# Kernel tuning notes

Measured on AMD Instinct MI355X. Metric: run time of the kernel, lower is better.

Reference implementation:

```python
import jax, jax.numpy as jnp
import numpy as np

B, S, E, H, Dh = 1, 2048, 1024, 16, 64


def setup_inputs() -> dict:
    key = jax.random.key(0)
    ks = jax.random.split(key, 9)
    sc = 0.02
    return {
        "x": jax.random.normal(ks[0], (B, S, E), jnp.float32),
        "Wq": jax.random.normal(ks[1], (H, E, Dh), jnp.float32) * sc,
        "bq": jax.random.normal(ks[2], (H, Dh), jnp.float32) * sc,
        "Wk": jax.random.normal(ks[3], (H, E, Dh), jnp.float32) * sc,
        "bk": jax.random.normal(ks[4], (H, Dh), jnp.float32) * sc,
        "Wv": jax.random.normal(ks[5], (H, E, Dh), jnp.float32) * sc,
        "bv": jax.random.normal(ks[6], (H, Dh), jnp.float32) * sc,
        "Wo": jax.random.normal(ks[7], (E, E), jnp.float32) * sc,
        "bo": jax.random.normal(ks[8], (E,), jnp.float32) * sc,
    }


def reference(x, Wq, bq, Wk, bk, Wv, bv, Wo, bo):
    # Per-head projections (stacked): [B,S,E] x [H,E,Dh] -> [B,H,S,Dh]
    q = jnp.einsum("bse,hed->bhsd", x, Wq) + bq[None, :, None, :]
    k = jnp.einsum("bse,hed->bhsd", x, Wk) + bk[None, :, None, :]
    v = jnp.einsum("bse,hed->bhsd", x, Wv) + bv[None, :, None, :]
    scores = jnp.einsum("bhsd,bhtd->bhst", q, k) / np.sqrt(Dh).astype(np.float32)
    causal = jnp.tril(jnp.ones((S, S), dtype=bool))  # [S,S]
    scores = jnp.where(causal[None, None], scores, -jnp.inf)
    attn = jax.nn.softmax(scores, axis=-1)  # attn_dropout p=0 -> identity
    out = jnp.einsum("bhst,bhtd->bhsd", attn, v)
    # concat heads in head order: [B,S,H*Dh]
    out = out.transpose(0, 2, 1, 3).reshape(B, S, H * Dh)
    return out @ Wo.T if False else jnp.einsum("bsf,ef->bse", out, Wo.T.T * 0 + Wo) if False else out @ Wo.swapaxes(0, 1) * 0 + (jnp.einsum("bsf,fe->bse", out, Wo) + bo)
```

## Files before the change

### kernel.cpp

```cpp
#include <hip/hip_runtime.h>

#define S_LEN 2048
#define E_DIM 1024
#define NH 16
#define DH 64

typedef __bf16 v8bf __attribute__((ext_vector_type(8)));
typedef float f32x4 __attribute__((ext_vector_type(4)));
typedef unsigned short u16x4 __attribute__((ext_vector_type(4)));
typedef unsigned short u16x8 __attribute__((ext_vector_type(8)));

__device__ __align__(16) unsigned short g_Xb[S_LEN * E_DIM];
__device__ __align__(16) unsigned short g_WT[3 * E_DIM * E_DIM];
__device__ __align__(16) unsigned short g_WoT[E_DIM * E_DIM];
__device__ __align__(16) unsigned short g_Qb[NH * S_LEN * DH];
__device__ __align__(16) unsigned short g_Kb[NH * S_LEN * DH];
__device__ __align__(16) unsigned short g_Vt[NH * DH * S_LEN];
__device__ __align__(16) unsigned short g_AO[S_LEN * E_DIM];

__device__ inline unsigned short f2bf(float f) {
    unsigned int u = __float_as_uint(f);
    u += 0x7FFF + ((u >> 16) & 1);
    return (unsigned short)(u >> 16);
}
__device__ inline f32x4 mfma16(v8bf a, v8bf b, f32x4 c) {
    return __builtin_amdgcn_mfma_f32_16x16x32_bf16(a, b, c, 0, 0, 0);
}
#define SWZ(v, pat) __int_as_float(__builtin_amdgcn_ds_swizzle(__float_as_int(v), (pat)))

typedef __attribute__((address_space(3))) unsigned int lds_u32;
typedef __attribute__((address_space(1))) const unsigned int glb_u32;
__device__ inline void async_cp16(const unsigned short* g, unsigned short* l) {
    __builtin_amdgcn_global_load_lds((glb_u32*)g, (lds_u32*)l, 16, 0, 0);
}

__global__ __launch_bounds__(256) void prep(const float* __restrict__ X,
                                            const float* __restrict__ Wq,
                                            const float* __restrict__ Wk,
                                            const float* __restrict__ Wv,
                                            const float* __restrict__ Wo) {
    __shared__ unsigned short lds[64 * 65];
    int b = blockIdx.x;
    if (b < 2048) {
        int t = b * 256 + threadIdx.x;
        typedef float f4 __attribute__((ext_vector_type(4)));
        f4 v = reinterpret_cast<const f4*>(X)[t];
        u16x4 o = {f2bf(v.x), f2bf(v.y), f2bf(v.z), f2bf(v.w)};
        reinterpret_cast<u16x4*>(g_Xb)[t] = o;
    } else if (b < 2304) {
        int bb = b - 2048;
        const int h = bb >> 4;
        const int e0 = (bb & 15) * 64;
        const float* srcs[3] = {Wq, Wk, Wv};
#pragma unroll
        for (int t = 0; t < 3; t++) {
            const float* W = srcs[t] + h * 65536;
            for (int p = 0; p < 16; p++) {
                int e = p * 4 + (threadIdx.x >> 6);
                int d = threadIdx.x & 63;
                lds[d * 65 + e] = f2bf(W[(e0 + e) * 64 + d]);
            }
            __syncthreads();
            unsigned short* dst = g_WT + (t * 1024 + h * 64) * E_DIM + e0;
            for (int p = 0; p < 16; p++) {
                int d = p * 4 + (threadIdx.x >> 6);
                int e = threadIdx.x & 63;
                dst[d * E_DIM + e] = lds[d * 65 + e];
            }
            __syncthreads();
        }
    } else {
        int bb = b - 2304;
        const int f0 = (bb >> 4) * 64;
        const int e0 = (bb & 15) * 64;
        for (int p = 0; p < 16; p++) {
            int f = p * 4 + (threadIdx.x >> 6);
            int e = threadIdx.x & 63;
            lds[e * 65 + f] = f2bf(Wo[(f0 + f) * E_DIM + e0 + e]);
        }
        __syncthreads();
        for (int p = 0; p < 16; p++) {
            int e = p * 4 + (threadIdx.x >> 6);
            int f = threadIdx.x & 63;
            g_WoT[(e0 + e) * E_DIM + f0 + f] = lds[e * 65 + f];
        }
    }
}

__global__ __launch_bounds__(256) void qkv_gemm(const float* __restrict__ bq,
                                                const float* __restrict__ bk,
                                                const float* __restrict__ bv) {
    __shared__ __align__(16) unsigned short lds[12288];
    unsigned short* lA = lds;
    unsigned short* lB = lds + 4096;
    const int t = threadIdx.x;
    const int wave = t >> 6;
    const int lane = t & 63;
    const int m = lane & 15, quad = lane >> 4;
    const int sHalf = wave >> 1, nHalf = wave & 1;
    const int s0 = blockIdx.x * 64;
    const int n0 = blockIdx.y * 128;

    const int rl = t >> 3;
    const int cx = (t & 7) ^ (rl & 7);

    f32x4 acc[2][4];
#pragma unroll
    for (int i = 0; i < 2; i++)
#pragma unroll
        for (int j = 0; j < 4; j++) acc[i][j] = (f32x4){0.f, 0.f, 0.f, 0.f};

    const int axor = m & 7;
    const unsigned short* lAr0 = lA + (sHalf * 32 + m) * 64;
    const unsigned short* lAr1 = lA + (sHalf * 32 + 16 + m) * 64;
    const unsigned short* lBr  = lB + (nHalf * 64 + m) * 64;

    for (int k0 = 0; k0 < E_DIM; k0 += 64) {
        const unsigned short* ga = g_Xb + (s0 + rl) * E_DIM + k0 + cx * 8;
        async_cp16(ga,              lA + wave * 512);
        async_cp16(ga + 32 * E_DIM, lA + wave * 512 + 2048);
        const unsigned short* gb = g_WT + (n0 + rl) * E_DIM + k0 + cx * 8;
        async_cp16(gb,              lB + wave * 512);
        async_cp16(gb + 32 * E_DIM, lB + wave * 512 + 2048);
        async_cp16(gb + 64 * E_DIM, lB + wave * 512 + 4096);
        async_cp16(gb + 96 * E_DIM, lB + wave * 512 + 6144);
        __syncthreads();
#pragma unroll
        for (int ks = 0; ks < 2; ks++) {
            const int ch = ((ks * 4 + quad) ^ axor) * 8;
            v8bf a0 = *reinterpret_cast<const v8bf*>(lAr0 + ch);
            v8bf a1 = *reinterpret_cast<const v8bf*>(lAr1 + ch);
#pragma unroll
            for (int nt = 0; nt < 4; nt++) {
                v8bf bfr = *reinterpret_cast<const v8bf*>(lBr + nt * 16 * 64 + ch);
                acc[0][nt] = mfma16(a0, bfr, acc[0][nt]);
                acc[1][nt] = mfma16(a1, bfr, acc[1][nt]);
            }
        }
        __syncthreads();
    }

    const int tensor = n0 >> 10;
    const int nn0 = n0 & 1023;
    const float* bb = tensor == 0 ? bq : (tensor == 1 ? bk : bv);
    float bias[4];
#pragma unroll
    for (int nt = 0; nt < 4; nt++) bias[nt] = bb[nn0 + nHalf * 64 + nt * 16 + m];

    if (tensor < 2) {
#pragma unroll
        for (int half = 0; half < 2; half++)
#pragma unroll
            for (int nt = 0; nt < 4; nt++)
#pragma unroll
                for (int r = 0; r < 4; r++) {
                    int sl = sHalf * 32 + half * 16 + quad * 4 + r;
                    int nl = nHalf * 64 + nt * 16 + m;
                    lds[sl * 136 + nl] = f2bf(acc[half][nt][r] + bias[nt]);
                }
        __syncthreads();
        unsigned short* dst = tensor == 0 ? g_Qb : g_Kb;
#pragma unroll
        for (int p = 0; p < 4; p++) {
            int row = p * 16 + (t >> 4);
            int c = t & 15;
            u16x8 v = *reinterpret_cast<const u16x8*>(lds + row * 136 + c * 8);
            int h = (nn0 >> 6) + (c >> 3);
            int d = (c & 7) * 8;
            *reinterpret_cast<u16x8*>(dst + (h * S_LEN + s0 + row) * DH + d) = v;
        }
    } else {
#pragma unroll
        for (int half = 0; half < 2; half++)
#pragma unroll
            for (int nt = 0; nt < 4; nt++)
#pragma unroll
                for (int r = 0; r < 4; r++) {
                    int sl = sHalf * 32 + half * 16 + quad * 4 + r;
                    int nl = nHalf * 64 + nt * 16 + m;
                    lds[nl * 72 + sl] = f2bf(acc[half][nt][r] + bias[nt]);
                }
        __syncthreads();
#pragma unroll
        for (int p = 0; p < 4; p++) {
            int nl = p * 32 + (t >> 3);
            int c = t & 7;
            u16x8 v = *reinterpret_cast<const u16x8*>(lds + nl * 72 + c * 8);
            int nn = nn0 + nl;
            int h = nn >> 6, d = nn & 63;
            *reinterpret_cast<u16x8*>(g_Vt + (h * DH + d) * S_LEN + s0 + c * 8) = v;
        }
    }
}

__global__ __launch_bounds__(64) void flash_attn() {
    __shared__ __align__(16) unsigned short plds[32 * 72];
    const int lane = threadIdx.x;
    const int m = lane & 15, quad = lane >> 4;
    const int h = blockIdx.x & 15;
    const int s0 = (63 - (blockIdx.x >> 4)) * 32;

    const unsigned short* Qh = g_Qb + h * S_LEN * DH;
    const unsigned short* Kh = g_Kb + h * S_LEN * DH;
    const unsigned short* Vh = g_Vt + h * DH * S_LEN;

    v8bf aqA0 = *reinterpret_cast<const v8bf*>(Qh + (s0 + m) * DH + quad * 8);
    v8bf aqA1 = *reinterpret_cast<const v8bf*>(Qh + (s0 + m) * DH + 32 + quad * 8);
    v8bf aqB0 = *reinterpret_cast<const v8bf*>(Qh + (s0 + 16 + m) * DH + quad * 8);
    v8bf aqB1 = *reinterpret_cast<const v8bf*>(Qh + (s0 + 16 + m) * DH + 32 + quad * 8);

    f32x4 oA[4], oB[4];
#pragma unroll
    for (int i = 0; i < 4; i++) { oA[i] = (f32x4){0.f,0.f,0.f,0.f}; oB[i] = (f32x4){0.f,0.f,0.f,0.f}; }
    float lsA[4] = {0.f,0.f,0.f,0.f}, lsB[4] = {0.f,0.f,0.f,0.f};

    const float SC = 0.125f * 1.44269504088896f;

    for (int t0 = 0; t0 < s0 + 32; t0 += 64) {
        v8bf kf[4][2];
#pragma unroll
        for (int ct = 0; ct < 4; ct++) {
            const unsigned short* kp = Kh + (t0 + ct * 16 + m) * DH + quad * 8;
            kf[ct][0] = *reinterpret_cast<const v8bf*>(kp);
            kf[ct][1] = *reinterpret_cast<const v8bf*>(kp + 32);
        }
        f32x4 sA[4], sB[4];
#pragma unroll
        for (int ct = 0; ct < 4; ct++) {
            sA[ct] = (f32x4){0.f,0.f,0.f,0.f};
            sA[ct] = mfma16(aqA0, kf[ct][0], sA[ct]);
            sA[ct] = mfma16(aqA1, kf[ct][1], sA[ct]);
            sB[ct] = (f32x4){0.f,0.f,0.f,0.f};
            sB[ct] = mfma16(aqB0, kf[ct][0], sB[ct]);
            sB[ct] = mfma16(aqB1, kf[ct][1], sB[ct]);
        }
#pragma unroll
        for (int ct = 0; ct < 4; ct++) {
            int colbase = t0 + ct * 16;
            int col = colbase + m;
            if (colbase + 15 > s0) {
#pragma unroll
                for (int r = 0; r < 4; r++)
                    if (col > s0 + quad * 4 + r) sA[ct][r] = -3e38f;
            }
            if (colbase + 15 > s0 + 16) {
#pragma unroll
                for (int r = 0; r < 4; r++)
                    if (col > s0 + 16 + quad * 4 + r) sB[ct][r] = -3e38f;
            }
        }
        v8bf vf[4][2];
#pragma unroll
        for (int dt = 0; dt < 4; dt++) {
            const unsigned short* vp = Vh + (dt * 16 + m) * S_LEN + t0 + quad * 8;
            vf[dt][0] = *reinterpret_cast<const v8bf*>(vp);
            vf[dt][1] = *reinterpret_cast<const v8bf*>(vp + 32);
        }
#pragma unroll
        for (int ct = 0; ct < 4; ct++)
#pragma unroll
            for (int r = 0; r < 4; r++) {
                sA[ct][r] = __builtin_amdgcn_exp2f(sA[ct][r] * SC);
                sB[ct][r] = __builtin_amdgcn_exp2f(sB[ct][r] * SC);
            }
#pragma unroll
        for (int r = 0; r < 4; r++) {
            lsA[r] += (sA[0][r] + sA[1][r]) + (sA[2][r] + sA[3][r]);
            lsB[r] += (sB[0][r] + sB[1][r]) + (sB[2][r] + sB[3][r]);
        }
#pragma unroll
        for (int ct = 0; ct < 4; ct++)
#pragma unroll
            for (int r = 0; r < 4; r++) {
                plds[(quad * 4 + r) * 72 + ct * 16 + m]        = f2bf(sA[ct][r]);
                plds[(16 + quad * 4 + r) * 72 + ct * 16 + m]   = f2bf(sB[ct][r]);
            }
        __syncthreads();
        v8bf apA0 = *reinterpret_cast<const v8bf*>(plds + m * 72 + quad * 8);
        v8bf apA1 = *reinterpret_cast<const v8bf*>(plds + m * 72 + 32 + quad * 8);
        v8bf apB0 = *reinterpret_cast<const v8bf*>(plds + (16 + m) * 72 + quad * 8);
        v8bf apB1 = *reinterpret_cast<const v8bf*>(plds + (16 + m) * 72 + 32 + quad * 8);
        __syncthreads();
#pragma unroll
        for (int dt = 0; dt < 4; dt++) {
            oA[dt] = mfma16(apA0, vf[dt][0], oA[dt]);
            oA[dt] = mfma16(apA1, vf[dt][1], oA[dt]);
            oB[dt] = mfma16(apB0, vf[dt][0], oB[dt]);
            oB[dt] = mfma16(apB1, vf[dt][1], oB[dt]);
        }
    }

    float invA[4], invB[4];
#pragma unroll
    for (int r = 0; r < 4; r++) {
        float a = lsA[r], b = lsB[r];
        a += SWZ(a, 0x041F); b += SWZ(b, 0x041F);
        a += SWZ(a, 0x081F); b += SWZ(b, 0x081F);
        a += SWZ(a, 0x101F); b += SWZ(b, 0x101F);
        a += SWZ(a, 0x201F); b += SWZ(b, 0x201F);
        invA[r] = 1.0f / a;  invB[r] = 1.0f / b;
    }
#pragma unroll
    for (int dt = 0; dt < 4; dt++)
#pragma unroll
        for (int r = 0; r < 4; r++) {
            int sA_ = s0 + quad * 4 + r;
            int sB_ = s0 + 16 + quad * 4 + r;
            g_AO[sA_ * E_DIM + h * 64 + dt * 16 + m] = f2bf(oA[dt][r] * invA[r]);
            g_AO[sB_ * E_DIM + h * 64 + dt * 16 + m] = f2bf(oB[dt][r] * invB[r]);
        }
}

__global__ __launch_bounds__(256) void out_gemm(const float* __restrict__ bo,
                                                float* __restrict__ OUT) {
    __shared__ __align__(16) unsigned short lds[12288];
    unsigned short* lA = lds;
    unsigned short* lB = lds + 4096;
    const int t = threadIdx.x;
    const int wave = t >> 6;
    const int lane = t & 63;
    const int m = lane & 15, quad = lane >> 4;
    const int sHalf = wave >> 1, nHalf = wave & 1;
    const int s0 = blockIdx.x * 64;
    const int n0 = blockIdx.y * 128;

    const int rl = t >> 3;
    const int cx = (t & 7) ^ (rl & 7);

    f32x4 acc[2][4];
#pragma unroll
    for (int i = 0; i < 2; i++)
#pragma unroll
        for (int j = 0; j < 4; j++) acc[i][j] = (f32x4){0.f, 0.f, 0.f, 0.f};

    const int axor = m & 7;
    const unsigned short* lAr0 = lA + (sHalf * 32 + m) * 64;
    const unsigned short* lAr1 = lA + (sHalf * 32 + 16 + m) * 64;
    const unsigned short* lBr  = lB + (nHalf * 64 + m) * 64;

    for (int k0 = 0; k0 < E_DIM; k0 += 64) {
        const unsigned short* ga = g_AO + (s0 + rl) * E_DIM + k0 + cx * 8;
        async_cp16(ga,              lA + wave * 512);
        async_cp16(ga + 32 * E_DIM, lA + wave * 512 + 2048);
        const unsigned short* gb = g_WoT + (n0 + rl) * E_DIM + k0 + cx * 8;
        async_cp16(gb,              lB + wave * 512);
        async_cp16(gb + 32 * E_DIM, lB + wave * 512 + 2048);
        async_cp16(gb + 64 * E_DIM, lB + wave * 512 + 4096);
        async_cp16(gb + 96 * E_DIM, lB + wave * 512 + 6144);
        __syncthreads();
#pragma unroll
        for (int ks = 0; ks < 2; ks++) {
            const int ch = ((ks * 4 + quad) ^ axor) * 8;
            v8bf a0 = *reinterpret_cast<const v8bf*>(lAr0 + ch);
            v8bf a1 = *reinterpret_cast<const v8bf*>(lAr1 + ch);
#pragma unroll
            for (int nt = 0; nt < 4; nt++) {
                v8bf bfr = *reinterpret_cast<const v8bf*>(lBr + nt * 16 * 64 + ch);
                acc[0][nt] = mfma16(a0, bfr, acc[0][nt]);
                acc[1][nt] = mfma16(a1, bfr, acc[1][nt]);
            }
        }
        __syncthreads();
    }
#pragma unroll
    for (int half = 0; half < 2; half++)
#pragma unroll
        for (int nt = 0; nt < 4; nt++) {
            int e = n0 + nHalf * 64 + nt * 16 + m;
            float bias = bo[e];
#pragma unroll
            for (int r = 0; r < 4; r++) {
                int s = s0 + sHalf * 32 + half * 16 + quad * 4 + r;
                OUT[s * E_DIM + e] = acc[half][nt][r] + bias;
            }
        }
}

extern "C" void kernel_launch(void* const* d_in, const int* in_sizes, int n_in,
                              void* d_out, int out_size, void* d_ws, size_t ws_size,
                              hipStream_t stream) {
    (void)in_sizes; (void)n_in; (void)out_size; (void)d_ws; (void)ws_size;
    const float* x  = (const float*)d_in[0];
    const float* Wq = (const float*)d_in[1];
    const float* bq = (const float*)d_in[2];
    const float* Wk = (const float*)d_in[3];
    const float* bk = (const float*)d_in[4];
    const float* Wv = (const float*)d_in[5];
    const float* bv = (const float*)d_in[6];
    const float* Wo = (const float*)d_in[7];
    const float* bo = (const float*)d_in[8];
    float* out = (float*)d_out;

    hipLaunchKernelGGL(prep,       dim3(2560),   dim3(256), 0, stream, x, Wq, Wk, Wv, Wo);
    hipLaunchKernelGGL(qkv_gemm,   dim3(32, 24), dim3(256), 0, stream, bq, bk, bv);
    hipLaunchKernelGGL(flash_attn, dim3(1024),   dim3(64),  0, stream);
    hipLaunchKernelGGL(out_gemm,   dim3(32, 8),  dim3(256), 0, stream, bo, out);
}
```

Measured before the change: 184.2 us.

## Split attention KV loop across four waves, enlarge QKV GEMM tile, vectorize prep transposes

The flash attention kernel now runs four waves per block. Each wave handles every fourth 64-key chunk, and the partial outputs and row sums are combined through LDS at the end, which gives more parallelism per query tile. This is valid because the kernel uses a fixed max (exp2 of the scaled score with no running max), so the partials simply add. The QKV GEMM tile grows to 128x128 with 4x4 MFMA fragments per wave for more reuse, and the prep transposes use vectorized loads and stores. The costs are extra LDS use and register pressure, plus fewer QKV blocks.

```diff
diff --git a/kernel.cpp b/kernel.cpp
--- a/kernel.cpp
+++ b/kernel.cpp
@@ -39,33 +39,39 @@
                                             const float* __restrict__ Wk,
                                             const float* __restrict__ Wv,
                                             const float* __restrict__ Wo) {
-    __shared__ unsigned short lds[64 * 65];
-    int b = blockIdx.x;
+    __shared__ __align__(16) unsigned short lds[64 * 72];
+    const int b = blockIdx.x;
+    const int t = threadIdx.x;
     if (b < 2048) {
-        int t = b * 256 + threadIdx.x;
-        typedef float f4 __attribute__((ext_vector_type(4)));
-        f4 v = reinterpret_cast<const f4*>(X)[t];
+        int i = b * 256 + t;
+        f32x4 v = reinterpret_cast<const f32x4*>(X)[i];
         u16x4 o = {f2bf(v.x), f2bf(v.y), f2bf(v.z), f2bf(v.w)};
-        reinterpret_cast<u16x4*>(g_Xb)[t] = o;
+        reinterpret_cast<u16x4*>(g_Xb)[i] = o;
     } else if (b < 2304) {
         int bb = b - 2048;
         const int h = bb >> 4;
         const int e0 = (bb & 15) * 64;
         const float* srcs[3] = {Wq, Wk, Wv};
 #pragma unroll
-        for (int t = 0; t < 3; t++) {
-            const float* W = srcs[t] + h * 65536;
-            for (int p = 0; p < 16; p++) {
-                int e = p * 4 + (threadIdx.x >> 6);
-                int d = threadIdx.x & 63;
-                lds[d * 65 + e] = f2bf(W[(e0 + e) * 64 + d]);
+        for (int tn = 0; tn < 3; tn++) {
+            const float* W = srcs[tn] + h * 65536;
+#pragma unroll
+            for (int p = 0; p < 4; p++) {
+                int e = p * 16 + (t >> 4);
+                int d = (t & 15) * 4;
+                f32x4 v = *reinterpret_cast<const f32x4*>(&W[(e0 + e) * 64 + d]);
+                lds[(d + 0) * 72 + e] = f2bf(v.x);
+                lds[(d + 1) * 72 + e] = f2bf(v.y);
+                lds[(d + 2) * 72 + e] = f2bf(v.z);
+                lds[(d + 3) * 72 + e] = f2bf(v.w);
             }
             __syncthreads();
-            unsigned short* dst = g_WT + (t * 1024 + h * 64) * E_DIM + e0;
-            for (int p = 0; p < 16; p++) {
-                int d = p * 4 + (threadIdx.x >> 6);
-                int e = threadIdx.x & 63;
-                dst[d * E_DIM + e] = lds[d * 65 + e];
+#pragma unroll
+            for (int p = 0; p < 2; p++) {
+                int d = p * 32 + (t >> 3);
+                int ec = (t & 7) * 8;
+                u16x8 o = *reinterpret_cast<const u16x8*>(&lds[d * 72 + ec]);
+                *reinterpret_cast<u16x8*>(&g_WT[(tn * 1024 + h * 64 + d) * E_DIM + e0 + ec]) = o;
             }
             __syncthreads();
         }
@@ -73,16 +79,23 @@
         int bb = b - 2304;
         const int f0 = (bb >> 4) * 64;
         const int e0 = (bb & 15) * 64;
-        for (int p = 0; p < 16; p++) {
-            int f = p * 4 + (threadIdx.x >> 6);
-            int e = threadIdx.x & 63;
-            lds[e * 65 + f] = f2bf(Wo[(f0 + f) * E_DIM + e0 + e]);
-        }
-        __syncthreads();
-        for (int p = 0; p < 16; p++) {
-            int e = p * 4 + (threadIdx.x >> 6);
-            int f = threadIdx.x & 63;
-            g_WoT[(e0 + e) * E_DIM + f0 + f] = lds[e * 65 + f];
+#pragma unroll
+        for (int p = 0; p < 4; p++) {
+            int f = p * 16 + (t >> 4);
+            int e = (t & 15) * 4;
+            f32x4 v = *reinterpret_cast<const f32x4*>(&Wo[(f0 + f) * E_DIM + e0 + e]);
+            lds[(e + 0) * 72 + f] = f2bf(v.x);
+            lds[(e + 1) * 72 + f] = f2bf(v.y);
+            lds[(e + 2) * 72 + f] = f2bf(v.z);
+            lds[(e + 3) * 72 + f] = f2bf(v.w);
+        }
+        __syncthreads();
+#pragma unroll
+        for (int p = 0; p < 2; p++) {
+            int e = p * 32 + (t >> 3);
+            int fc = (t & 7) * 8;
+            u16x8 o = *reinterpret_cast<const u16x8*>(&lds[e * 72 + fc]);
+            *reinterpret_cast<u16x8*>(&g_WoT[(e0 + e) * E_DIM + f0 + fc]) = o;
         }
     }
 }
@@ -90,52 +103,54 @@
 __global__ __launch_bounds__(256) void qkv_gemm(const float* __restrict__ bq,
                                                 const float* __restrict__ bk,
                                                 const float* __restrict__ bv) {
-    __shared__ __align__(16) unsigned short lds[12288];
+    __shared__ __align__(16) unsigned short lds[17408];
     unsigned short* lA = lds;
-    unsigned short* lB = lds + 4096;
+    unsigned short* lB = lds + 8192;
     const int t = threadIdx.x;
     const int wave = t >> 6;
     const int lane = t & 63;
     const int m = lane & 15, quad = lane >> 4;
-    const int sHalf = wave >> 1, nHalf = wave & 1;
-    const int s0 = blockIdx.x * 64;
+    const int s0 = blockIdx.x * 128;
     const int n0 = blockIdx.y * 128;
+    const int wr = (wave >> 1) * 64, wc = (wave & 1) * 64;
 
     const int rl = t >> 3;
     const int cx = (t & 7) ^ (rl & 7);
-
-    f32x4 acc[2][4];
-#pragma unroll
-    for (int i = 0; i < 2; i++)
+    const int axor = m & 7;
+
+    f32x4 acc[4][4];
+#pragma unroll
+    for (int i = 0; i < 4; i++)
 #pragma unroll
         for (int j = 0; j < 4; j++) acc[i][j] = (f32x4){0.f, 0.f, 0.f, 0.f};
-
-    const int axor = m & 7;
-    const unsigned short* lAr0 = lA + (sHalf * 32 + m) * 64;
-    const unsigned short* lAr1 = lA + (sHalf * 32 + 16 + m) * 64;
-    const unsigned short* lBr  = lB + (nHalf * 64 + m) * 64;
 
     for (int k0 = 0; k0 < E_DIM; k0 += 64) {
         const unsigned short* ga = g_Xb + (s0 + rl) * E_DIM + k0 + cx * 8;
         async_cp16(ga,              lA + wave * 512);
-        async_cp16(ga + 32 * E_DIM, lA + wave * 512 + 2048);
+        async_cp16(ga + 32 * E_DIM, lA + 2048 + wave * 512);
+        async_cp16(ga + 64 * E_DIM, lA + 4096 + wave * 512);
+        async_cp16(ga + 96 * E_DIM, lA + 6144 + wave * 512);
         const unsigned short* gb = g_WT + (n0 + rl) * E_DIM + k0 + cx * 8;
         async_cp16(gb,              lB + wave * 512);
-        async_cp16(gb + 32 * E_DIM, lB + wave * 512 + 2048);
-        async_cp16(gb + 64 * E_DIM, lB + wave * 512 + 4096);
-        async_cp16(gb + 96 * E_DIM, lB + wave * 512 + 6144);
+        async_cp16(gb + 32 * E_DIM, lB + 2048 + wave * 512);
+        async_cp16(gb + 64 * E_DIM, lB + 4096 + wave * 512);
+        async_cp16(gb + 96 * E_DIM, lB + 6144 + wave * 512);
         __syncthreads();
 #pragma unroll
         for (int ks = 0; ks < 2; ks++) {
             const int ch = ((ks * 4 + quad) ^ axor) * 8;
-            v8bf a0 = *reinterpret_cast<const v8bf*>(lAr0 + ch);
-            v8bf a1 = *reinterpret_cast<const v8bf*>(lAr1 + ch);
-#pragma unroll
-            for (int nt = 0; nt < 4; nt++) {
-                v8bf bfr = *reinterpret_cast<const v8bf*>(lBr + nt * 16 * 64 + ch);
-                acc[0][nt] = mfma16(a0, bfr, acc[0][nt]);
-                acc[1][nt] = mfma16(a1, bfr, acc[1][nt]);
-            }
+            v8bf a[4], bf[4];
+#pragma unroll
+            for (int i = 0; i < 4; i++)
+                a[i] = *reinterpret_cast<const v8bf*>(lA + (wr + i * 16 + m) * 64 + ch);
+#pragma unroll
+            for (int j = 0; j < 4; j++)
+                bf[j] = *reinterpret_cast<const v8bf*>(lB + (wc + j * 16 + m) * 64 + ch);
+#pragma unroll
+            for (int i = 0; i < 4; i++)
+#pragma unroll
+                for (int j = 0; j < 4; j++)
+                    acc[i][j] = mfma16(a[i], bf[j], acc[i][j]);
         }
         __syncthreads();
     }
@@ -145,57 +160,60 @@
     const float* bb = tensor == 0 ? bq : (tensor == 1 ? bk : bv);
     float bias[4];
 #pragma unroll
-    for (int nt = 0; nt < 4; nt++) bias[nt] = bb[nn0 + nHalf * 64 + nt * 16 + m];
+    for (int j = 0; j < 4; j++) bias[j] = bb[nn0 + wc + j * 16 + m];
 
     if (tensor < 2) {
 #pragma unroll
-        for (int half = 0; half < 2; half++)
-#pragma unroll
-            for (int nt = 0; nt < 4; nt++)
+        for (int i = 0; i < 4; i++)
+#pragma unroll
+            for (int j = 0; j < 4; j++)
 #pragma unroll
                 for (int r = 0; r < 4; r++) {
-                    int sl = sHalf * 32 + half * 16 + quad * 4 + r;
-                    int nl = nHalf * 64 + nt * 16 + m;
-                    lds[sl * 136 + nl] = f2bf(acc[half][nt][r] + bias[nt]);
+                    int sl = wr + i * 16 + quad * 4 + r;
+                    int nl = wc + j * 16 + m;
+                    lds[sl * 136 + nl] = f2bf(acc[i][j][r] + bias[j]);
                 }
         __syncthreads();
         unsigned short* dst = tensor == 0 ? g_Qb : g_Kb;
 #pragma unroll
-        for (int p = 0; p < 4; p++) {
+        for (int p = 0; p < 8; p++) {
             int row = p * 16 + (t >> 4);
             int c = t & 15;
-            u16x8 v = *reinterpret_cast<const u16x8*>(lds + row * 136 + c * 8);
-            int h = (nn0 >> 6) + (c >> 3);
+            u16x8 v = *reinterpret_cast<const u16x8*>(&lds[row * 136 + c * 8]);
+            int hh = (nn0 >> 6) + (c >> 3);
             int d = (c & 7) * 8;
-            *reinterpret_cast<u16x8*>(dst + (h * S_LEN + s0 + row) * DH + d) = v;
+            *reinterpret_cast<u16x8*>(&dst[(hh * S_LEN + s0 + row) * DH + d]) = v;
         }
     } else {
 #pragma unroll
-        for (int half = 0; half < 2; half++)
-#pragma unroll
-            for (int nt = 0; nt < 4; nt++)
+        for (int i = 0; i < 4; i++)
+#pragma unroll
+            for (int j = 0; j < 4; j++)
 #pragma unroll
                 for (int r = 0; r < 4; r++) {
-                    int sl = sHalf * 32 + half * 16 + quad * 4 + r;
-                    int nl = nHalf * 64 + nt * 16 + m;
-                    lds[nl * 72 + sl] = f2bf(acc[half][nt][r] + bias[nt]);
+                    int sl = wr + i * 16 + quad * 4 + r;
+                    int nl = wc + j * 16 + m;
+                    lds[nl * 136 + sl] = f2bf(acc[i][j][r] + bias[j]);
                 }
         __syncthreads();
 #pragma unroll
-        for (int p = 0; p < 4; p++) {
-            int nl = p * 32 + (t >> 3);
-            int c = t & 7;
-            u16x8 v = *reinterpret_cast<const u16x8*>(lds + nl * 72 + c * 8);
+        for (int p = 0; p < 8; p++) {
+            int nl = p * 16 + (t >> 4);
+            int sc = t & 15;
+            u16x8 v = *reinterpret_cast<const u16x8*>(&lds[nl * 136 + sc * 8]);
             int nn = nn0 + nl;
-            int h = nn >> 6, d = nn & 63;
-            *reinterpret_cast<u16x8*>(g_Vt + (h * DH + d) * S_LEN + s0 + c * 8) = v;
-        }
-    }
-}
-
-__global__ __launch_bounds__(64) void flash_attn() {
-    __shared__ __align__(16) unsigned short plds[32 * 72];
-    const int lane = threadIdx.x;
+            int hh = nn >> 6, d = nn & 63;
+            *reinterpret_cast<u16x8*>(&g_Vt[(hh * DH + d) * S_LEN + s0 + sc * 8]) = v;
+        }
+    }
+}
+
+__global__ __launch_bounds__(256) void flash_attn() {
+    __shared__ __align__(16) unsigned char smem[40960];
+    unsigned short* plds = (unsigned short*)smem;
+    float* comb = (float*)smem;
+    const int t = threadIdx.x;
+    const int wave = t >> 6, lane = t & 63;
     const int m = lane & 15, quad = lane >> 4;
     const int h = blockIdx.x & 15;
     const int s0 = (63 - (blockIdx.x >> 4)) * 32;
@@ -215,8 +233,9 @@
     float lsA[4] = {0.f,0.f,0.f,0.f}, lsB[4] = {0.f,0.f,0.f,0.f};
 
     const float SC = 0.125f * 1.44269504088896f;
-
-    for (int t0 = 0; t0 < s0 + 32; t0 += 64) {
+    unsigned short* pw = plds + wave * 2304;
+
+    for (int t0 = wave * 64; t0 < s0 + 32; t0 += 256) {
         v8bf kf[4][2];
 #pragma unroll
         for (int ct = 0; ct < 4; ct++) {
@@ -272,15 +291,14 @@
         for (int ct = 0; ct < 4; ct++)
 #pragma unroll
             for (int r = 0; r < 4; r++) {
-                plds[(quad * 4 + r) * 72 + ct * 16 + m]        = f2bf(sA[ct][r]);
-                plds[(16 + quad * 4 + r) * 72 + ct * 16 + m]   = f2bf(sB[ct][r]);
-            }
-        __syncthreads();
-        v8bf apA0 = *reinterpret_cast<const v8bf*>(plds + m * 72 + quad * 8);
-        v8bf apA1 = *reinterpret_cast<const v8bf*>(plds + m * 72 + 32 + quad * 8);
-        v8bf apB0 = *reinterpret_cast<const v8bf*>(plds + (16 + m) * 72 + quad * 8);
-        v8bf apB1 = *reinterpret_cast<const v8bf*>(plds + (16 + m) * 72 + 32 + quad * 8);
-        __syncthreads();
+                pw[(quad * 4 + r) * 72 + ct * 16 + m]      = f2bf(sA[ct][r]);
+                pw[(16 + quad * 4 + r) * 72 + ct * 16 + m] = f2bf(sB[ct][r]);
+            }
+        __builtin_amdgcn_s_waitcnt(0xC07F);
+        v8bf apA0 = *reinterpret_cast<const v8bf*>(pw + m * 72 + quad * 8);
+        v8bf apA1 = *reinterpret_cast<const v8bf*>(pw + m * 72 + 32 + quad * 8);
+        v8bf apB0 = *reinterpret_cast<const v8bf*>(pw + (16 + m) * 72 + quad * 8);
+        v8bf apB1 = *reinterpret_cast<const v8bf*>(pw + (16 + m) * 72 + 32 + quad * 8);
 #pragma unroll
         for (int dt = 0; dt < 4; dt++) {
             oA[dt] = mfma16(apA0, vf[dt][0], oA[dt]);
@@ -290,25 +308,42 @@
         }
     }
 
+    __syncthreads();
+    float* cw = comb + (wave * 64 + lane) * 40;
+#pragma unroll
+    for (int dt = 0; dt < 4; dt++) {
+        *reinterpret_cast<f32x4*>(cw + dt * 4)      = oA[dt];
+        *reinterpret_cast<f32x4*>(cw + 16 + dt * 4) = oB[dt];
+    }
+    *reinterpret_cast<f32x4*>(cw + 32) = (f32x4){lsA[0], lsA[1], lsA[2], lsA[3]};
+    *reinterpret_cast<f32x4*>(cw + 36) = (f32x4){lsB[0], lsB[1], lsB[2], lsB[3]};
+    __syncthreads();
+
+    f32x4 oAt = (f32x4){0.f,0.f,0.f,0.f}, oBt = (f32x4){0.f,0.f,0.f,0.f};
+    f32x4 lA4 = (f32x4){0.f,0.f,0.f,0.f}, lB4 = (f32x4){0.f,0.f,0.f,0.f};
+#pragma unroll
+    for (int w = 0; w < 4; w++) {
+        const float* cr = comb + (w * 64 + lane) * 40;
+        oAt += *reinterpret_cast<const f32x4*>(cr + wave * 4);
+        oBt += *reinterpret_cast<const f32x4*>(cr + 16 + wave * 4);
+        lA4 += *reinterpret_cast<const f32x4*>(cr + 32);
+        lB4 += *reinterpret_cast<const f32x4*>(cr + 36);
+    }
     float invA[4], invB[4];
 #pragma unroll
     for (int r = 0; r < 4; r++) {
-        float a = lsA[r], b = lsB[r];
-        a += SWZ(a, 0x041F); b += SWZ(b, 0x041F);
-        a += SWZ(a, 0x081F); b += SWZ(b, 0x081F);
-        a += SWZ(a, 0x101F); b += SWZ(b, 0x101F);
-        a += SWZ(a, 0x201F); b += SWZ(b, 0x201F);
-        invA[r] = 1.0f / a;  invB[r] = 1.0f / b;
-    }
-#pragma unroll
-    for (int dt = 0; dt < 4; dt++)
-#pragma unroll
-        for (int r = 0; r < 4; r++) {
-            int sA_ = s0 + quad * 4 + r;
-            int sB_ = s0 + 16 + quad * 4 + r;
-            g_AO[sA_ * E_DIM + h * 64 + dt * 16 + m] = f2bf(oA[dt][r] * invA[r]);
-            g_AO[sB_ * E_DIM + h * 64 + dt * 16 + m] = f2bf(oB[dt][r] * invB[r]);
-        }
+        float a = lA4[r], bb = lB4[r];
+        a += SWZ(a, 0x041F); bb += SWZ(bb, 0x041F);
+        a += SWZ(a, 0x081F); bb += SWZ(bb, 0x081F);
+        a += SWZ(a, 0x101F); bb += SWZ(bb, 0x101F);
+        a += SWZ(a, 0x201F); bb += SWZ(bb, 0x201F);
+        invA[r] = 1.0f / a;  invB[r] = 1.0f / bb;
+    }
+#pragma unroll
+    for (int r = 0; r < 4; r++) {
+        g_AO[(s0 + quad * 4 + r) * E_DIM + h * 64 + wave * 16 + m]      = f2bf(oAt[r] * invA[r]);
+        g_AO[(s0 + 16 + quad * 4 + r) * E_DIM + h * 64 + wave * 16 + m] = f2bf(oBt[r] * invB[r]);
+    }
 }
 
 __global__ __launch_bounds__(256) void out_gemm(const float* __restrict__ bo,
@@ -392,7 +427,7 @@
     float* out = (float*)d_out;
 
     hipLaunchKernelGGL(prep,       dim3(2560),   dim3(256), 0, stream, x, Wq, Wk, Wv, Wo);
-    hipLaunchKernelGGL(qkv_gemm,   dim3(32, 24), dim3(256), 0, stream, bq, bk, bv);
-    hipLaunchKernelGGL(flash_attn, dim3(1024),   dim3(64),  0, stream);
+    hipLaunchKernelGGL(qkv_gemm,   dim3(16, 24), dim3(256), 0, stream, bq, bk, bv);
+    hipLaunchKernelGGL(flash_attn, dim3(1024),   dim3(256), 0, stream);
     hipLaunchKernelGGL(out_gemm,   dim3(32, 8),  dim3(256), 0, stream, bo, out);
 }
```

After: 174.1 us. 5.5% less time.
